# Optimization experiments

Measured on AMD Instinct MI355X. Metric: run time of the kernel, lower is better.

## Reference

```python
import jax, jax.numpy as jnp
import numpy as np

K = 128      # knowledge_n (= net1 = prednet output width)
LOW = 64     # low_dim
PP = 64      # pp_dim
STU = 50000  # student_n
EXER = 20000 # exer_n
S_RANGES = [(0, 9999), (10000, 19999)]
NR = len(S_RANGES)
B = 4096


def setup_inputs() -> dict:
    key = jax.random.key(0)
    ks = jax.random.split(key, 16)

    def xavier(k, shape):
        fan_in, fan_out = shape[-1], shape[-2] if len(shape) > 1 else shape[-1]
        lim = np.sqrt(6.0 / (fan_in + fan_out))
        return jax.random.uniform(k, shape, jnp.float32, -lim, lim)

    return {
        "stu_id": jax.random.randint(ks[0], (B,), 0, STU),
        "exer_id": jax.random.randint(ks[1], (B,), 0, EXER),
        "kn_emb": jnp.ones((B, K), jnp.float32),
        "student_emb": xavier(ks[2], (NR, STU, LOW)),          # ParameterList stacked
        "prompt_stu": xavier(ks[3], (STU, PP)),
        "knowledge_emb": jax.random.normal(ks[4], (K, LOW), jnp.float32),
        "k_difficulty": xavier(ks[5], (EXER, LOW)),
        "s_exer_vectors": jax.random.uniform(ks[6], (NR, PP), jnp.float32),
        "W1": xavier(ks[7], (K, K + LOW)),                      # prednet_full1 (no bias)
        "W2": xavier(ks[8], (K, K + LOW)),                      # prednet_full2 (no bias)
        "W3": xavier(ks[9], (1, K)),                            # prednet_full3
        "b3": jnp.zeros((1,), jnp.float32),
        "fc1_W": xavier(ks[10], (K, PP + K)),
        "fc1_b": jnp.zeros((K,), jnp.float32),
        "fc2_W": xavier(ks[11], (K, PP + K)),
        "fc2_b": jnp.zeros((K,), jnp.float32),
    }


def reference(stu_id, exer_id, kn_emb, student_emb, prompt_stu, knowledge_emb,
              k_difficulty, s_exer_vectors, W1, W2, W3, b3, fc1_W, fc1_b, fc2_W, fc2_b):
    sig = jax.nn.sigmoid
    kle = knowledge_emb  # [K, LOW]

    # --- student side ---
    # prompt_stu.repeat(NR, 1) then index_select == index prompt_stu with stu_id % STU
    p_stu = prompt_stu[stu_id % STU]                              # [B, PP]
    stu_cat = student_emb.reshape(NR * STU, LOW)                  # concat of ParameterList
    old_stu = sig(stu_cat[stu_id] @ kle.T)                        # [B, K]
    stu_e = sig(jnp.concatenate([p_stu, old_stu], 1) @ fc1_W.T + fc1_b)  # [B, K]

    # --- exercise side ---
    counts = np.array([r[1] - r[0] + 1 for r in S_RANGES])
    temp_vectors = jnp.repeat(s_exer_vectors, counts, axis=0, total_repeat_length=EXER)
    p_exer = sig(temp_vectors[exer_id])                           # [B, PP]
    old_exer = sig(sig(k_difficulty[exer_id]) @ kle.T)            # [B, K]
    exer_e = sig(jnp.concatenate([p_exer, old_exer], 1) @ fc2_W.T + fc2_b)  # [B, K]

    # --- per-concept interaction ---
    # cat([x_broadcast, kn_vector], 2) @ W.T splits into x @ Wa.T + kle @ Wb.T
    W1a, W1b = W1[:, :K], W1[:, K:]
    W2a, W2b = W2[:, :K], W2[:, K:]
    preference = sig((stu_e @ W1a.T)[:, None, :] + (kle @ W1b.T)[None, :, :])   # [B, K, K]
    diff = sig((exer_e @ W2a.T)[:, None, :] + (kle @ W2b.T)[None, :, :])        # [B, K, K]

    o = sig((preference - diff) @ W3.T + b3)                      # [B, K, 1]
    sum_out = jnp.sum(o * kn_emb[:, :, None], axis=1)             # [B, 1]
    count = jnp.sum(kn_emb, axis=1, keepdims=True)
    return sum_out / count
```

## Files before the change

kernel.cpp:

```cpp
#include <hip/hip_runtime.h>
#include <hip/hip_bf16.h>

#define STUN   50000
#define BATCH  4096
#define LOG2E  1.4426950408889634f

__device__ __forceinline__ float fexp2(float x){ return __builtin_amdgcn_exp2f(x); }
__device__ __forceinline__ float frcp (float x){ return __builtin_amdgcn_rcpf(x); }
__device__ __forceinline__ float fsig (float x){ return frcp(1.0f + fexp2(-LOG2E * x)); }

__global__ __launch_bounds__(128) void k_pre(
    const float* __restrict__ kle,
    const float* __restrict__ W1,
    const float* __restrict__ W2,
    const float* __restrict__ fc1_W,
    const float* __restrict__ fc2_W,
    float* __restrict__ kle4,
    float* __restrict__ fc1i,
    float* __restrict__ fc2i,
    float* __restrict__ W1ai,
    float* __restrict__ W2ai,
    float* __restrict__ E1i,
    float* __restrict__ E2i)
{
    const int bid = blockIdx.x;
    const int t   = threadIdx.x;
    if (bid < 16) {
        const int u4 = bid;
        float4 v;
        v.x = kle[t * 64 + u4 * 4 + 0];
        v.y = kle[t * 64 + u4 * 4 + 1];
        v.z = kle[t * 64 + u4 * 4 + 2];
        v.w = kle[t * 64 + u4 * 4 + 3];
        *(float4*)&kle4[(u4 * 128 + t) * 4] = v;
    } else if (bid < 64) {
        const int u4 = bid - 16;
        float4 v;
        v.x = fc1_W[t * 192 + u4 * 4 + 0];
        v.y = fc1_W[t * 192 + u4 * 4 + 1];
        v.z = fc1_W[t * 192 + u4 * 4 + 2];
        v.w = fc1_W[t * 192 + u4 * 4 + 3];
        *(float4*)&fc1i[(u4 * 128 + t) * 4] = v;
    } else if (bid < 112) {
        const int u4 = bid - 64;
        float4 v;
        v.x = fc2_W[t * 192 + u4 * 4 + 0];
        v.y = fc2_W[t * 192 + u4 * 4 + 1];
        v.z = fc2_W[t * 192 + u4 * 4 + 2];
        v.w = fc2_W[t * 192 + u4 * 4 + 3];
        *(float4*)&fc2i[(u4 * 128 + t) * 4] = v;
    } else if (bid < 144) {
        const int u4 = bid - 112;
        float4 v;
        v.x = W1[t * 192 + u4 * 4 + 0];
        v.y = W1[t * 192 + u4 * 4 + 1];
        v.z = W1[t * 192 + u4 * 4 + 2];
        v.w = W1[t * 192 + u4 * 4 + 3];
        *(float4*)&W1ai[(u4 * 128 + t) * 4] = v;
    } else if (bid < 176) {
        const int u4 = bid - 144;
        float4 v;
        v.x = W2[t * 192 + u4 * 4 + 0];
        v.y = W2[t * 192 + u4 * 4 + 1];
        v.z = W2[t * 192 + u4 * 4 + 2];
        v.w = W2[t * 192 + u4 * 4 + 3];
        *(float4*)&W2ai[(u4 * 128 + t) * 4] = v;
    } else if (bid < 304) {
        const int j = bid - 176;
        float acc = 0.f;
        #pragma unroll
        for (int u4 = 0; u4 < 16; ++u4) {
            const float4 kv = *(const float4*)&kle[t * 64 + u4 * 4];
            const float4 wv = *(const float4*)&W1[j * 192 + 128 + u4 * 4];
            acc += kv.x * wv.x + kv.y * wv.y + kv.z * wv.z + kv.w * wv.w;
        }
        E1i[((j >> 2) * 128 + t) * 4 + (j & 3)] = fexp2(-LOG2E * acc);
    } else {
        const int j = bid - 304;
        float acc = 0.f;
        #pragma unroll
        for (int u4 = 0; u4 < 16; ++u4) {
            const float4 kv = *(const float4*)&kle[t * 64 + u4 * 4];
            const float4 wv = *(const float4*)&W2[j * 192 + 128 + u4 * 4];
            acc += kv.x * wv.x + kv.y * wv.y + kv.z * wv.z + kv.w * wv.w;
        }
        E2i[((j >> 2) * 128 + t) * 4 + (j & 3)] = fexp2(-LOG2E * acc);
    }
}

__global__ __launch_bounds__(256, 6) void k_fused(
    const int*   __restrict__ stu_id,
    const int*   __restrict__ exer_id,
    const float* __restrict__ student_emb,
    const float* __restrict__ prompt_stu,
    const float* __restrict__ k_diff,
    const float* __restrict__ s_exer,
    const float* __restrict__ kle4,
    const float* __restrict__ fc1i,
    const float* __restrict__ fc2i,
    const float* __restrict__ W1ai,
    const float* __restrict__ W2ai,
    const float* __restrict__ fc1_b,
    const float* __restrict__ fc2_b,
    const float* __restrict__ E1i,
    const float* __restrict__ E2i,
    const float* __restrict__ W3,
    const float* __restrict__ b3,
    const float* __restrict__ kn,
    float* __restrict__ out)
{
    __shared__ __align__(16) float sh_in [4][64][4];
    __shared__ __align__(16) float sh_old[2][128][4];
    __shared__ __align__(16) float sh_e  [2][128][4];
    __shared__ __align__(16) float ses   [2][4][128];
    __shared__ float sW3[128];
    __shared__ __align__(16) float redj[2][64][4];
    __shared__ float red2_o[2][4];
    __shared__ float red2_k[2][4];

    const int t  = threadIdx.x;
    const int b0 = blockIdx.x * 4;

    {
        const int g   = t >> 6;
        const int u   = t & 63;
        const int sid = stu_id[b0 + g];
        const int eid = exer_id[b0 + g];
        const int er  = (eid >= 10000) ? 1 : 0;
        sh_in[0][u][g] = student_emb[sid * 64 + u];
        sh_in[1][u][g] = fsig(k_diff[eid * 64 + u]);
        sh_in[2][u][g] = prompt_stu[(sid % STUN) * 64 + u];
        sh_in[3][u][g] = fsig(s_exer[er * 64 + u]);
    }
    if (t < 32) *(float4*)&sW3[t * 4] = *(const float4*)&W3[t * 4];
    __syncthreads();

    const int half = t >> 7;
    const int idx  = t & 127;

    float acc[4];

#define FMA4(xbase) { \
        const float4 x0 = *(const float4*)&(xbase)[0]; \
        acc[0] += wv * x0.x; acc[1] += wv * x0.y; acc[2] += wv * x0.z; acc[3] += wv * x0.w; }

#define WSTEP(WARR, XARR, u4) { \
        const float4 w4 = *(const float4*)&WARR[((u4) * 128 + idx) * 4]; \
        { const float wv = w4.x; FMA4(XARR[(u4)*4+0]); } \
        { const float wv = w4.y; FMA4(XARR[(u4)*4+1]); } \
        { const float wv = w4.z; FMA4(XARR[(u4)*4+2]); } \
        { const float wv = w4.w; FMA4(XARR[(u4)*4+3]); } }

#define WSTEPO(WARR, XARR, u4, uoff) { \
        const float4 w4 = *(const float4*)&WARR[((u4) * 128 + idx) * 4]; \
        { const float wv = w4.x; FMA4(XARR[((u4)-(uoff))*4+0]); } \
        { const float wv = w4.y; FMA4(XARR[((u4)-(uoff))*4+1]); } \
        { const float wv = w4.z; FMA4(XARR[((u4)-(uoff))*4+2]); } \
        { const float wv = w4.w; FMA4(XARR[((u4)-(uoff))*4+3]); } }

    #pragma unroll
    for (int b = 0; b < 4; ++b) acc[b] = 0.f;
    #pragma unroll 4
    for (int u4 = 0; u4 < 16; ++u4) WSTEP(kle4, sh_in[half], u4);
    #pragma unroll
    for (int b = 0; b < 4; ++b) sh_old[half][idx][b] = fsig(acc[b]);
    __syncthreads();

    {
        const float* fcT = half ? fc2i : fc1i;
        #pragma unroll
        for (int b = 0; b < 4; ++b) acc[b] = 0.f;
        #pragma unroll 4
        for (int u4 = 0; u4 < 16; ++u4) WSTEP(fcT, sh_in[2 + half], u4);
        #pragma unroll 4
        for (int u4 = 16; u4 < 48; ++u4) WSTEPO(fcT, sh_old[half], u4, 16);
        const float bias = (half ? fc2_b : fc1_b)[idx];
        #pragma unroll
        for (int b = 0; b < 4; ++b) sh_e[half][idx][b] = fsig(acc[b] + bias);
    }
    __syncthreads();

    {
        const float* WT = half ? W2ai : W1ai;
        #pragma unroll
        for (int b = 0; b < 4; ++b) acc[b] = 0.f;
        #pragma unroll 4
        for (int u4 = 0; u4 < 32; ++u4) WSTEP(WT, sh_e[half], u4);
        #pragma unroll
        for (int b = 0; b < 4; ++b)
            ses[half][b][idx] = fexp2(-LOG2E * acc[b]);
    }
#undef FMA4
#undef WSTEP
#undef WSTEPO
    __syncthreads();

    const int w   = t >> 6;
    const int kk  = t & 63;
    const int kh  = w & 1;
    const int jh  = w >> 1;
    const int k2  = kh * 64 + kk;

    const float4* E1v = (const float4*)E1i;
    const float4* E2v = (const float4*)E2i;

    float ac0 = 0.f, ac1 = 0.f, ac2 = 0.f, ac3 = 0.f;

#define COMP(acc, esv1, esv2, e1c, e2c, w3c) { \
        const float uu = (esv1) * (e1c); \
        const float vv = (esv2) * (e2c); \
        const float dd = frcp((1.f + uu) * (1.f + vv)); \
        acc += ((vv - uu) * dd) * (w3c); }

    #pragma unroll 2
    for (int j4 = 0; j4 < 16; ++j4) {
        const int jj4 = jh * 16 + j4;
        const int j   = jj4 * 4;
        const float4 e1 = E1v[jj4 * 128 + k2];
        const float4 e2 = E2v[jj4 * 128 + k2];
        const float4 w3 = *(const float4*)&sW3[j];

#define BODY(acc, bi) { \
        const float4 s1 = *(const float4*)&ses[0][bi][j]; \
        const float4 s2 = *(const float4*)&ses[1][bi][j]; \
        COMP(acc, s1.x, s2.x, e1.x, e2.x, w3.x); \
        COMP(acc, s1.y, s2.y, e1.y, e2.y, w3.y); \
        COMP(acc, s1.z, s2.z, e1.z, e2.z, w3.z); \
        COMP(acc, s1.w, s2.w, e1.w, e2.w, w3.w); }

        BODY(ac0, 0);
        BODY(ac1, 1);
        BODY(ac2, 2);
        BODY(ac3, 3);
#undef BODY
    }
#undef COMP

    if (jh == 1) {
        redj[kh][kk][0] = ac0; redj[kh][kk][1] = ac1;
        redj[kh][kk][2] = ac2; redj[kh][kk][3] = ac3;
    }
    __syncthreads();
    if (jh == 0) {
        const float bb3 = b3[0];
        const float4 other = *(const float4*)&redj[kh][kk][0];
        float to[4] = { ac0 + other.x, ac1 + other.y, ac2 + other.z, ac3 + other.w };
        float co[4], ck[4];
        #pragma unroll
        for (int i = 0; i < 4; ++i) {
            const float o   = fsig(to[i] + bb3);
            const float knv = kn[(b0 + i) * 128 + k2];
            co[i] = o * knv;
            ck[i] = knv;
        }
        #pragma unroll
        for (int off = 1; off < 64; off <<= 1) {
            #pragma unroll
            for (int i = 0; i < 4; ++i) {
                co[i] += __shfl_xor(co[i], off);
                ck[i] += __shfl_xor(ck[i], off);
            }
        }
        if (kk == 0) {
            #pragma unroll
            for (int i = 0; i < 4; ++i) {
                red2_o[kh][i] = co[i];
                red2_k[kh][i] = ck[i];
            }
        }
    }
    __syncthreads();
    if (t < 4) {
        const float so = red2_o[0][t] + red2_o[1][t];
        const float sk = red2_k[0][t] + red2_k[1][t];
        out[b0 + t] = so / sk;
    }
}

extern "C" void kernel_launch(void* const* d_in, const int* in_sizes, int n_in,
                              void* d_out, int out_size, void* d_ws, size_t ws_size,
                              hipStream_t stream)
{
    const int*   stu_id      = (const int*)  d_in[0];
    const int*   exer_id     = (const int*)  d_in[1];
    const float* kn_emb      = (const float*)d_in[2];
    const float* student_emb = (const float*)d_in[3];
    const float* prompt_stu  = (const float*)d_in[4];
    const float* kle         = (const float*)d_in[5];
    const float* k_diff      = (const float*)d_in[6];
    const float* s_exer      = (const float*)d_in[7];
    const float* W1          = (const float*)d_in[8];
    const float* W2          = (const float*)d_in[9];
    const float* W3          = (const float*)d_in[10];
    const float* b3          = (const float*)d_in[11];
    const float* fc1_W       = (const float*)d_in[12];
    const float* fc1_b       = (const float*)d_in[13];
    const float* fc2_W       = (const float*)d_in[14];
    const float* fc2_b       = (const float*)d_in[15];
    float* out = (float*)d_out;

    float* ws   = (float*)d_ws;
    float* kle4 = ws;
    float* fc1i = kle4 + 8192;
    float* fc2i = fc1i + 24576;
    float* W1ai = fc2i + 24576;
    float* W2ai = W1ai + 16384;
    float* E1i  = W2ai + 16384;
    float* E2i  = E1i  + 16384;

    k_pre<<<432, 128, 0, stream>>>(kle, W1, W2, fc1_W, fc2_W,
                                   kle4, fc1i, fc2i, W1ai, W2ai, E1i, E2i);
    k_fused<<<BATCH / 4, 256, 0, stream>>>(stu_id, exer_id, student_emb, prompt_stu,
                                           k_diff, s_exer, kle4, fc1i, fc2i,
                                           W1ai, W2ai, fc1_b, fc2_b,
                                           E1i, E2i, W3, b3, kn_emb, out);
}
```

Baseline: 55.13 us.

## Split fused kernel into per-stage kernels with global intermediates

Breaks the single fused batch kernel into six launches: gather, old embedding, fc layer, W-a projection, the pairwise interaction, and the final reduction. Each stage writes its result to workspace buffers in global memory instead of shared memory. This removes block-level syncs and lets each stage use smaller blocks with more grid parallelism. The cost is extra kernel launches and global memory round trips for the intermediates.

```diff
diff --git a/kernel.cpp b/kernel.cpp
--- a/kernel.cpp
+++ b/kernel.cpp
@@ -88,193 +88,236 @@
     }
 }
 
-__global__ __launch_bounds__(256, 6) void k_fused(
+__global__ __launch_bounds__(512) void k_g(
     const int*   __restrict__ stu_id,
     const int*   __restrict__ exer_id,
     const float* __restrict__ student_emb,
     const float* __restrict__ prompt_stu,
     const float* __restrict__ k_diff,
     const float* __restrict__ s_exer,
+    float* __restrict__ xg)
+{
+    const int t = threadIdx.x;
+    const int b = blockIdx.x * 8 + (t >> 6);
+    const int u = t & 63;
+    const int sid = stu_id[b];
+    const int eid = exer_id[b];
+    const int er  = (eid >= 10000) ? 1 : 0;
+    float* xb = xg + b * 256;
+    xb[u]       = student_emb[sid * 64 + u];
+    xb[64 + u]  = fsig(k_diff[eid * 64 + u]);
+    xb[128 + u] = prompt_stu[(sid % STUN) * 64 + u];
+    xb[192 + u] = fsig(s_exer[er * 64 + u]);
+}
+
+#define STEP4(A, W, X) { \
+    A = fmaf((W).x, (X).x, A); A = fmaf((W).y, (X).y, A); \
+    A = fmaf((W).z, (X).z, A); A = fmaf((W).w, (X).w, A); }
+
+__global__ __launch_bounds__(128) void k_old(
+    const float* __restrict__ xg,
     const float* __restrict__ kle4,
+    float* __restrict__ old_g)
+{
+    const int half = blockIdx.x & 1;
+    const int b0   = (blockIdx.x >> 1) * 4;
+    const int idx  = threadIdx.x;
+    const float* xb0 = xg + (b0 + 0) * 256 + half * 64;
+    const float* xb1 = xg + (b0 + 1) * 256 + half * 64;
+    const float* xb2 = xg + (b0 + 2) * 256 + half * 64;
+    const float* xb3 = xg + (b0 + 3) * 256 + half * 64;
+    float a0 = 0.f, a1 = 0.f, a2 = 0.f, a3 = 0.f;
+    #pragma unroll 4
+    for (int u4 = 0; u4 < 16; ++u4) {
+        const float4 w  = *(const float4*)&kle4[(u4 * 128 + idx) * 4];
+        const float4 x0 = *(const float4*)&xb0[u4 * 4];
+        const float4 x1 = *(const float4*)&xb1[u4 * 4];
+        const float4 x2 = *(const float4*)&xb2[u4 * 4];
+        const float4 x3 = *(const float4*)&xb3[u4 * 4];
+        STEP4(a0, w, x0); STEP4(a1, w, x1); STEP4(a2, w, x2); STEP4(a3, w, x3);
+    }
+    const int o = half * 128 + idx;
+    old_g[(b0 + 0) * 256 + o] = fsig(a0);
+    old_g[(b0 + 1) * 256 + o] = fsig(a1);
+    old_g[(b0 + 2) * 256 + o] = fsig(a2);
+    old_g[(b0 + 3) * 256 + o] = fsig(a3);
+}
+
+__global__ __launch_bounds__(128) void k_e(
+    const float* __restrict__ xg,
+    const float* __restrict__ old_g,
     const float* __restrict__ fc1i,
     const float* __restrict__ fc2i,
+    const float* __restrict__ fc1_b,
+    const float* __restrict__ fc2_b,
+    float* __restrict__ e_g)
+{
+    const int half = blockIdx.x & 1;
+    const int b0   = (blockIdx.x >> 1) * 4;
+    const int idx  = threadIdx.x;
+    const float* fcT = half ? fc2i : fc1i;
+    const float* pb0 = xg + (b0 + 0) * 256 + 128 + half * 64;
+    const float* pb1 = xg + (b0 + 1) * 256 + 128 + half * 64;
+    const float* pb2 = xg + (b0 + 2) * 256 + 128 + half * 64;
+    const float* pb3 = xg + (b0 + 3) * 256 + 128 + half * 64;
+    const float* ob0 = old_g + (b0 + 0) * 256 + half * 128;
+    const float* ob1 = old_g + (b0 + 1) * 256 + half * 128;
+    const float* ob2 = old_g + (b0 + 2) * 256 + half * 128;
+    const float* ob3 = old_g + (b0 + 3) * 256 + half * 128;
+    float a0 = 0.f, a1 = 0.f, a2 = 0.f, a3 = 0.f;
+    #pragma unroll 4
+    for (int u4 = 0; u4 < 16; ++u4) {
+        const float4 w  = *(const float4*)&fcT[(u4 * 128 + idx) * 4];
+        const float4 x0 = *(const float4*)&pb0[u4 * 4];
+        const float4 x1 = *(const float4*)&pb1[u4 * 4];
+        const float4 x2 = *(const float4*)&pb2[u4 * 4];
+        const float4 x3 = *(const float4*)&pb3[u4 * 4];
+        STEP4(a0, w, x0); STEP4(a1, w, x1); STEP4(a2, w, x2); STEP4(a3, w, x3);
+    }
+    #pragma unroll 4
+    for (int u4 = 16; u4 < 48; ++u4) {
+        const float4 w  = *(const float4*)&fcT[(u4 * 128 + idx) * 4];
+        const float4 x0 = *(const float4*)&ob0[(u4 - 16) * 4];
+        const float4 x1 = *(const float4*)&ob1[(u4 - 16) * 4];
+        const float4 x2 = *(const float4*)&ob2[(u4 - 16) * 4];
+        const float4 x3 = *(const float4*)&ob3[(u4 - 16) * 4];
+        STEP4(a0, w, x0); STEP4(a1, w, x1); STEP4(a2, w, x2); STEP4(a3, w, x3);
+    }
+    const float bias = (half ? fc2_b : fc1_b)[idx];
+    const int o = half * 128 + idx;
+    e_g[(b0 + 0) * 256 + o] = fsig(a0 + bias);
+    e_g[(b0 + 1) * 256 + o] = fsig(a1 + bias);
+    e_g[(b0 + 2) * 256 + o] = fsig(a2 + bias);
+    e_g[(b0 + 3) * 256 + o] = fsig(a3 + bias);
+}
+
+__global__ __launch_bounds__(128) void k_es(
+    const float* __restrict__ e_g,
     const float* __restrict__ W1ai,
     const float* __restrict__ W2ai,
-    const float* __restrict__ fc1_b,
-    const float* __restrict__ fc2_b,
+    float* __restrict__ es_g)
+{
+    const int half = blockIdx.x & 1;
+    const int b0   = (blockIdx.x >> 1) * 4;
+    const int idx  = threadIdx.x;
+    const float* WT  = half ? W2ai : W1ai;
+    const float* eb0 = e_g + (b0 + 0) * 256 + half * 128;
+    const float* eb1 = e_g + (b0 + 1) * 256 + half * 128;
+    const float* eb2 = e_g + (b0 + 2) * 256 + half * 128;
+    const float* eb3 = e_g + (b0 + 3) * 256 + half * 128;
+    float a0 = 0.f, a1 = 0.f, a2 = 0.f, a3 = 0.f;
+    #pragma unroll 4
+    for (int u4 = 0; u4 < 32; ++u4) {
+        const float4 w  = *(const float4*)&WT[(u4 * 128 + idx) * 4];
+        const float4 x0 = *(const float4*)&eb0[u4 * 4];
+        const float4 x1 = *(const float4*)&eb1[u4 * 4];
+        const float4 x2 = *(const float4*)&eb2[u4 * 4];
+        const float4 x3 = *(const float4*)&eb3[u4 * 4];
+        STEP4(a0, w, x0); STEP4(a1, w, x1); STEP4(a2, w, x2); STEP4(a3, w, x3);
+    }
+    const int o = half * 128 + idx;
+    es_g[(b0 + 0) * 256 + o] = fexp2(-LOG2E * a0);
+    es_g[(b0 + 1) * 256 + o] = fexp2(-LOG2E * a1);
+    es_g[(b0 + 2) * 256 + o] = fexp2(-LOG2E * a2);
+    es_g[(b0 + 3) * 256 + o] = fexp2(-LOG2E * a3);
+}
+
+__global__ __launch_bounds__(128) void k_mainp(
+    const float* __restrict__ es_g,
     const float* __restrict__ E1i,
     const float* __restrict__ E2i,
     const float* __restrict__ W3,
-    const float* __restrict__ b3,
-    const float* __restrict__ kn,
-    float* __restrict__ out)
-{
-    __shared__ __align__(16) float sh_in [4][64][4];
-    __shared__ __align__(16) float sh_old[2][128][4];
-    __shared__ __align__(16) float sh_e  [2][128][4];
-    __shared__ __align__(16) float ses   [2][4][128];
-    __shared__ float sW3[128];
-    __shared__ __align__(16) float redj[2][64][4];
-    __shared__ float red2_o[2][4];
-    __shared__ float red2_k[2][4];
-
-    const int t  = threadIdx.x;
-    const int b0 = blockIdx.x * 4;
-
-    {
-        const int g   = t >> 6;
-        const int u   = t & 63;
-        const int sid = stu_id[b0 + g];
-        const int eid = exer_id[b0 + g];
-        const int er  = (eid >= 10000) ? 1 : 0;
-        sh_in[0][u][g] = student_emb[sid * 64 + u];
-        sh_in[1][u][g] = fsig(k_diff[eid * 64 + u]);
-        sh_in[2][u][g] = prompt_stu[(sid % STUN) * 64 + u];
-        sh_in[3][u][g] = fsig(s_exer[er * 64 + u]);
-    }
-    if (t < 32) *(float4*)&sW3[t * 4] = *(const float4*)&W3[t * 4];
-    __syncthreads();
-
-    const int half = t >> 7;
-    const int idx  = t & 127;
-
-    float acc[4];
-
-#define FMA4(xbase) { \
-        const float4 x0 = *(const float4*)&(xbase)[0]; \
-        acc[0] += wv * x0.x; acc[1] += wv * x0.y; acc[2] += wv * x0.z; acc[3] += wv * x0.w; }
-
-#define WSTEP(WARR, XARR, u4) { \
-        const float4 w4 = *(const float4*)&WARR[((u4) * 128 + idx) * 4]; \
-        { const float wv = w4.x; FMA4(XARR[(u4)*4+0]); } \
-        { const float wv = w4.y; FMA4(XARR[(u4)*4+1]); } \
-        { const float wv = w4.z; FMA4(XARR[(u4)*4+2]); } \
-        { const float wv = w4.w; FMA4(XARR[(u4)*4+3]); } }
-
-#define WSTEPO(WARR, XARR, u4, uoff) { \
-        const float4 w4 = *(const float4*)&WARR[((u4) * 128 + idx) * 4]; \
-        { const float wv = w4.x; FMA4(XARR[((u4)-(uoff))*4+0]); } \
-        { const float wv = w4.y; FMA4(XARR[((u4)-(uoff))*4+1]); } \
-        { const float wv = w4.z; FMA4(XARR[((u4)-(uoff))*4+2]); } \
-        { const float wv = w4.w; FMA4(XARR[((u4)-(uoff))*4+3]); } }
-
-    #pragma unroll
-    for (int b = 0; b < 4; ++b) acc[b] = 0.f;
-    #pragma unroll 4
-    for (int u4 = 0; u4 < 16; ++u4) WSTEP(kle4, sh_in[half], u4);
-    #pragma unroll
-    for (int b = 0; b < 4; ++b) sh_old[half][idx][b] = fsig(acc[b]);
-    __syncthreads();
-
-    {
-        const float* fcT = half ? fc2i : fc1i;
-        #pragma unroll
-        for (int b = 0; b < 4; ++b) acc[b] = 0.f;
-        #pragma unroll 4
-        for (int u4 = 0; u4 < 16; ++u4) WSTEP(fcT, sh_in[2 + half], u4);
-        #pragma unroll 4
-        for (int u4 = 16; u4 < 48; ++u4) WSTEPO(fcT, sh_old[half], u4, 16);
-        const float bias = (half ? fc2_b : fc1_b)[idx];
-        #pragma unroll
-        for (int b = 0; b < 4; ++b) sh_e[half][idx][b] = fsig(acc[b] + bias);
-    }
-    __syncthreads();
-
-    {
-        const float* WT = half ? W2ai : W1ai;
-        #pragma unroll
-        for (int b = 0; b < 4; ++b) acc[b] = 0.f;
-        #pragma unroll 4
-        for (int u4 = 0; u4 < 32; ++u4) WSTEP(WT, sh_e[half], u4);
-        #pragma unroll
-        for (int b = 0; b < 4; ++b)
-            ses[half][b][idx] = fexp2(-LOG2E * acc[b]);
-    }
-#undef FMA4
-#undef WSTEP
-#undef WSTEPO
-    __syncthreads();
-
-    const int w   = t >> 6;
-    const int kk  = t & 63;
-    const int kh  = w & 1;
-    const int jh  = w >> 1;
-    const int k2  = kh * 64 + kk;
-
-    const float4* E1v = (const float4*)E1i;
-    const float4* E2v = (const float4*)E2i;
-
-    float ac0 = 0.f, ac1 = 0.f, ac2 = 0.f, ac3 = 0.f;
-
-#define COMP(acc, esv1, esv2, e1c, e2c, w3c) { \
-        const float uu = (esv1) * (e1c); \
-        const float vv = (esv2) * (e2c); \
+    float* __restrict__ accg)
+{
+    const int jh = blockIdx.x & 1;
+    const int b0 = (blockIdx.x >> 1) * 4;
+    const int k  = threadIdx.x;
+    const float4* E1v = (const float4*)E1i + jh * 16 * 128 + k;
+    const float4* E2v = (const float4*)E2i + jh * 16 * 128 + k;
+    const float* s1b0 = es_g + (b0 + 0) * 256 + jh * 64;
+    const float* s1b1 = es_g + (b0 + 1) * 256 + jh * 64;
+    const float* s1b2 = es_g + (b0 + 2) * 256 + jh * 64;
+    const float* s1b3 = es_g + (b0 + 3) * 256 + jh * 64;
+    const float* s2b0 = s1b0 + 128;
+    const float* s2b1 = s1b1 + 128;
+    const float* s2b2 = s1b2 + 128;
+    const float* s2b3 = s1b3 + 128;
+    const float* w3p  = W3 + jh * 64;
+
+    float a0 = 0.f, a1 = 0.f, a2 = 0.f, a3 = 0.f;
+
+#define COMP(acc, s1c, s2c, e1c, e2c, w3c) { \
+        const float uu = (s1c) * (e1c); \
+        const float vv = (s2c) * (e2c); \
         const float dd = frcp((1.f + uu) * (1.f + vv)); \
-        acc += ((vv - uu) * dd) * (w3c); }
-
-    #pragma unroll 2
-    for (int j4 = 0; j4 < 16; ++j4) {
-        const int jj4 = jh * 16 + j4;
-        const int j   = jj4 * 4;
-        const float4 e1 = E1v[jj4 * 128 + k2];
-        const float4 e2 = E2v[jj4 * 128 + k2];
-        const float4 w3 = *(const float4*)&sW3[j];
-
-#define BODY(acc, bi) { \
-        const float4 s1 = *(const float4*)&ses[0][bi][j]; \
-        const float4 s2 = *(const float4*)&ses[1][bi][j]; \
+        acc = fmaf((vv - uu) * dd, (w3c), acc); }
+
+#define BODY(acc, S1, S2) { \
+        const float4 s1 = *(const float4*)&(S1)[j4 * 4]; \
+        const float4 s2 = *(const float4*)&(S2)[j4 * 4]; \
         COMP(acc, s1.x, s2.x, e1.x, e2.x, w3.x); \
         COMP(acc, s1.y, s2.y, e1.y, e2.y, w3.y); \
         COMP(acc, s1.z, s2.z, e1.z, e2.z, w3.z); \
         COMP(acc, s1.w, s2.w, e1.w, e2.w, w3.w); }
 
-        BODY(ac0, 0);
-        BODY(ac1, 1);
-        BODY(ac2, 2);
-        BODY(ac3, 3);
+    #pragma unroll 4
+    for (int j4 = 0; j4 < 16; ++j4) {
+        const float4 e1 = E1v[j4 * 128];
+        const float4 e2 = E2v[j4 * 128];
+        const float4 w3 = *(const float4*)&w3p[j4 * 4];
+        BODY(a0, s1b0, s2b0);
+        BODY(a1, s1b1, s2b1);
+        BODY(a2, s1b2, s2b2);
+        BODY(a3, s1b3, s2b3);
+    }
 #undef BODY
-    }
 #undef COMP
 
-    if (jh == 1) {
-        redj[kh][kk][0] = ac0; redj[kh][kk][1] = ac1;
-        redj[kh][kk][2] = ac2; redj[kh][kk][3] = ac3;
-    }
-    __syncthreads();
-    if (jh == 0) {
-        const float bb3 = b3[0];
-        const float4 other = *(const float4*)&redj[kh][kk][0];
-        float to[4] = { ac0 + other.x, ac1 + other.y, ac2 + other.z, ac3 + other.w };
-        float co[4], ck[4];
+    accg[((b0 + 0) * 2 + jh) * 128 + k] = a0;
+    accg[((b0 + 1) * 2 + jh) * 128 + k] = a1;
+    accg[((b0 + 2) * 2 + jh) * 128 + k] = a2;
+    accg[((b0 + 3) * 2 + jh) * 128 + k] = a3;
+}
+
+__global__ __launch_bounds__(128) void k_fin(
+    const float* __restrict__ accg,
+    const float* __restrict__ b3,
+    const float* __restrict__ kn,
+    float* __restrict__ out)
+{
+    __shared__ float r[2][4][2];
+    const int t  = threadIdx.x;
+    const int b0 = blockIdx.x * 4;
+    const float bb3 = b3[0];
+    float co[4], ck[4];
+    #pragma unroll
+    for (int i = 0; i < 4; ++i) {
+        const int b = b0 + i;
+        const float acc = accg[(b * 2 + 0) * 128 + t] + accg[(b * 2 + 1) * 128 + t];
+        const float o   = fsig(acc + bb3);
+        const float knv = kn[b * 128 + t];
+        co[i] = o * knv;
+        ck[i] = knv;
+    }
+    #pragma unroll
+    for (int off = 1; off < 64; off <<= 1) {
         #pragma unroll
         for (int i = 0; i < 4; ++i) {
-            const float o   = fsig(to[i] + bb3);
-            const float knv = kn[(b0 + i) * 128 + k2];
-            co[i] = o * knv;
-            ck[i] = knv;
+            co[i] += __shfl_xor(co[i], off);
+            ck[i] += __shfl_xor(ck[i], off);
         }
+    }
+    if ((t & 63) == 0) {
+        const int wid = t >> 6;
         #pragma unroll
-        for (int off = 1; off < 64; off <<= 1) {
-            #pragma unroll
-            for (int i = 0; i < 4; ++i) {
-                co[i] += __shfl_xor(co[i], off);
-                ck[i] += __shfl_xor(ck[i], off);
-            }
+        for (int i = 0; i < 4; ++i) {
+            r[wid][i][0] = co[i];
+            r[wid][i][1] = ck[i];
         }
-        if (kk == 0) {
-            #pragma unroll
-            for (int i = 0; i < 4; ++i) {
-                red2_o[kh][i] = co[i];
-                red2_k[kh][i] = ck[i];
-            }
-        }
     }
     __syncthreads();
-    if (t < 4) {
-        const float so = red2_o[0][t] + red2_o[1][t];
-        const float sk = red2_k[0][t] + red2_k[1][t];
-        out[b0 + t] = so / sk;
-    }
+    if (t < 4)
+        out[b0 + t] = (r[0][t][0] + r[1][t][0]) / (r[0][t][1] + r[1][t][1]);
 }
 
 extern "C" void kernel_launch(void* const* d_in, const int* in_sizes, int n_in,
@@ -299,19 +342,28 @@
     const float* fc2_b       = (const float*)d_in[15];
     float* out = (float*)d_out;
 
-    float* ws   = (float*)d_ws;
-    float* kle4 = ws;
-    float* fc1i = kle4 + 8192;
-    float* fc2i = fc1i + 24576;
-    float* W1ai = fc2i + 24576;
-    float* W2ai = W1ai + 16384;
-    float* E1i  = W2ai + 16384;
-    float* E2i  = E1i  + 16384;
-
-    k_pre<<<432, 128, 0, stream>>>(kle, W1, W2, fc1_W, fc2_W,
-                                   kle4, fc1i, fc2i, W1ai, W2ai, E1i, E2i);
-    k_fused<<<BATCH / 4, 256, 0, stream>>>(stu_id, exer_id, student_emb, prompt_stu,
-                                           k_diff, s_exer, kle4, fc1i, fc2i,
-                                           W1ai, W2ai, fc1_b, fc2_b,
-                                           E1i, E2i, W3, b3, kn_emb, out);
-}
+    float* ws    = (float*)d_ws;
+    float* kle4  = ws;
+    float* fc1i  = kle4  + 8192;
+    float* fc2i  = fc1i  + 24576;
+    float* W1ai  = fc2i  + 24576;
+    float* W2ai  = W1ai  + 16384;
+    float* E1i   = W2ai  + 16384;
+    float* E2i   = E1i   + 16384;
+    float* xg    = E2i   + 16384;
+    float* old_g = xg    + 1048576;
+    float* e_g   = old_g + 1048576;
+    float* es_g  = e_g   + 1048576;
+    float* accg  = es_g  + 1048576;
+
+    k_pre  <<<432, 128, 0, stream>>>(kle, W1, W2, fc1_W, fc2_W,
+                                     kle4, fc1i, fc2i, W1ai, W2ai, E1i, E2i);
+    k_g    <<<BATCH / 8, 512, 0, stream>>>(stu_id, exer_id, student_emb,
+                                           prompt_stu, k_diff, s_exer, xg);
+    k_old  <<<(BATCH / 4) * 2, 128, 0, stream>>>(xg, kle4, old_g);
+    k_e    <<<(BATCH / 4) * 2, 128, 0, stream>>>(xg, old_g, fc1i, fc2i,
+                                                 fc1_b, fc2_b, e_g);
+    k_es   <<<(BATCH / 4) * 2, 128, 0, stream>>>(e_g, W1ai, W2ai, es_g);
+    k_mainp<<<(BATCH / 4) * 2, 128, 0, stream>>>(es_g, E1i, E2i, W3, accg);
+    k_fin  <<<BATCH / 4, 128, 0, stream>>>(accg, b3, kn_emb, out);
+}
```

Result: slower. 86.31 us (+56.6%).
